# Optimization experiments

Measured on AMD Instinct MI355X. Metric: run time of the kernel, lower is better.

The kernel has to match this reference:

```python
import jax, jax.numpy as jnp
import numpy as np

EPS = 1e-5
MAX_NORM = 1.0 - EPS
K = 16
ALPHA = 0.1
TAU = 0.1  # softmax temperature in forward


def project(x):
    # enforce ||x|| < 1 on the Poincare ball
    n = jnp.clip(jnp.linalg.norm(x, axis=-1, keepdims=True), EPS, None)
    return x / jnp.maximum(n / MAX_NORM, 1.0)


def mobius_add(u, v):
    c = 1.0
    dot_uv = jnp.sum(u * v, axis=-1, keepdims=True)
    nu = jnp.clip(jnp.sum(u * u, axis=-1, keepdims=True), 0.0, MAX_NORM ** 2)
    nv = jnp.clip(jnp.sum(v * v, axis=-1, keepdims=True), 0.0, MAX_NORM ** 2)
    num = (1 + 2 * c * dot_uv + c * nv) * u + (1 - c * nu) * v
    den = 1 + 2 * c * dot_uv + c * c * nu * nv
    return project(num / jnp.clip(den, EPS, None))


def exp_map(x, v):
    # sqrt_c = 1
    vn = jnp.clip(jnp.linalg.norm(v, axis=-1, keepdims=True), EPS, None)
    second = jnp.tanh(vn / 2.0) * v / vn
    return mobius_add(x, second)


def poincare_cdist(q, mem):
    # q: [B, M], mem: [N, M] -> [B, N] geodesic distances (c=1)
    qn = jnp.clip(jnp.sum(q * q, axis=-1), 0.0, MAX_NORM ** 2)          # [B]
    mn = jnp.clip(jnp.sum(mem * mem, axis=-1), 0.0, MAX_NORM ** 2)      # [N]
    # ||q - m||^2 expanded via gram matrix (same math as diff-based form)
    dist_sq = jnp.clip(jnp.sum(q * q, axis=-1)[:, None] + jnp.sum(mem * mem, axis=-1)[None, :]
                       - 2.0 * q @ mem.T, 0.0, None)                     # [B, N]
    den = (1.0 - qn)[:, None] * (1.0 - mn)[None, :]
    x = 2.0 * dist_sq / jnp.clip(den, EPS, None)
    return jnp.arccosh(1.0 + x)


def layernorm(x, g, b):
    mu = jnp.mean(x, axis=-1, keepdims=True)
    var = jnp.mean((x - mu) ** 2, axis=-1, keepdims=True)
    return (x - mu) / jnp.sqrt(var + 1e-5) * g + b


def setup_inputs() -> dict:
    key = jax.random.key(0)
    ks = jax.random.split(key, 10)
    B, S, H, M, N = 32, 2048, 1024, 128, 500000
    hidden_states = jax.random.normal(ks[0], (B, S, H), dtype=jnp.float32)
    W1 = jax.random.normal(ks[1], (H, M), dtype=jnp.float32) * 0.02
    b1 = jnp.zeros((M,), dtype=jnp.float32)
    ln_g = jnp.ones((M,), dtype=jnp.float32)
    ln_b = jnp.zeros((M,), dtype=jnp.float32)
    W2 = jax.random.normal(ks[2], (M, M), dtype=jnp.float32) * 0.02
    b2 = jnp.zeros((M,), dtype=jnp.float32)
    q_origin = jnp.zeros((1, M), dtype=jnp.float32)
    memory = project(jax.random.normal(ks[3], (N, M), dtype=jnp.float32) * 0.3)
    Wp = jax.random.normal(ks[4], (M, H), dtype=jnp.float32) * 0.02
    bp = jnp.zeros((H,), dtype=jnp.float32)
    return {"hidden_states": hidden_states, "W1": W1, "b1": b1, "ln_g": ln_g,
            "ln_b": ln_b, "W2": W2, "b2": b2, "q_origin": q_origin,
            "memory": memory, "Wp": Wp, "bp": bp}


def reference(hidden_states, W1, b1, ln_g, ln_b, W2, b2, q_origin, memory, Wp, bp):
    B, S, H = hidden_states.shape
    # query network on mean-pooled hidden states
    pooled = jnp.mean(hidden_states, axis=1)                  # [B, H]
    h = pooled @ W1 + b1                                      # [B, M]
    h = jax.nn.gelu(layernorm(h, ln_g, ln_b), approximate=False)
    tangent = h @ W2 + b2                                     # [B, M]
    origin = project(jnp.broadcast_to(q_origin, (B, q_origin.shape[-1])))
    query = exp_map(origin, tangent)                          # [B, M] on ball
    # geodesic kNN over the memory bank
    dists = poincare_cdist(query, memory)                     # [B, N]
    neg_top, idx = jax.lax.top_k(-dists, K)                   # smallest K
    top_d = -neg_top                                          # [B, K]
    neighbors = memory[idx]                                   # [B, K, M]
    w = jax.nn.softmax(-top_d / TAU, axis=-1)                 # [B, K]
    retrieved = jnp.einsum('bk,bkm->bm', w, neighbors)        # [B, M]
    force = retrieved @ Wp + bp                               # [B, H]
    return hidden_states + ALPHA * force[:, None, :]
```

## Files before the change

### kernel.cpp

```cpp
#include <hip/hip_runtime.h>
#include <float.h>
#include <math.h>

#define B_ 32
#define S_ 2048
#define H_ 1024
#define M_ 128
#define N_ 500000
#define KK 16
#define KK2 32
#define ALPHA_ 0.1f
#define TAU_ 0.1f
#define EPS_ 1e-5f
#define MAX_NORM_ 0.99999f
#define MAXN2_ (MAX_NORM_ * MAX_NORM_)
#define SC_ 64
#define RPB_ 256
#define NBLK_ ((N_ + RPB_ - 1) / RPB_)
#define WIN_ 2048
#define NWIN_ ((N_ + WIN_ - 1) / WIN_)
#define NPAD_ (NWIN_ * WIN_)

typedef __attribute__((ext_vector_type(8))) short short8;
typedef __attribute__((ext_vector_type(4))) float f32x4;

__device__ __forceinline__ unsigned short to_bf16(float x) {
    unsigned u = __float_as_uint(x);
    return (unsigned short)((u + 0x7FFFu + ((u >> 16) & 1u)) >> 16);
}

__global__ __launch_bounds__(256) void k1_pool(const float* __restrict__ hid,
                                               float* __restrict__ pp) {
    int bid = blockIdx.x;
    int b = bid >> 6, sc = bid & 63;
    const float4* h4 = (const float4*)hid + (((size_t)(b * S_ + sc * (S_ / SC_))) << 8) + threadIdx.x;
    float4 a0 = {0.f, 0.f, 0.f, 0.f}, a1 = a0, a2 = a0, a3 = a0;
    #pragma unroll
    for (int s = 0; s < S_ / SC_; s += 4) {
        float4 v0 = h4[(size_t)(s + 0) << 8];
        float4 v1 = h4[(size_t)(s + 1) << 8];
        float4 v2 = h4[(size_t)(s + 2) << 8];
        float4 v3 = h4[(size_t)(s + 3) << 8];
        a0.x += v0.x; a0.y += v0.y; a0.z += v0.z; a0.w += v0.w;
        a1.x += v1.x; a1.y += v1.y; a1.z += v1.z; a1.w += v1.w;
        a2.x += v2.x; a2.y += v2.y; a2.z += v2.z; a2.w += v2.w;
        a3.x += v3.x; a3.y += v3.y; a3.z += v3.z; a3.w += v3.w;
    }
    float4 acc;
    acc.x = (a0.x + a1.x) + (a2.x + a3.x);
    acc.y = (a0.y + a1.y) + (a2.y + a3.y);
    acc.z = (a0.z + a1.z) + (a2.z + a3.z);
    acc.w = (a0.w + a1.w) + (a2.w + a3.w);
    ((float4*)pp)[(size_t)(b * SC_ + sc) * 256 + threadIdx.x] = acc;
}

__device__ __forceinline__ float bred256(float v, volatile float* red, int tid) {
    red[tid] = v;
    __syncthreads();
    if (tid < 64) {
        float x = red[tid] + red[tid + 64] + red[tid + 128] + red[tid + 192];
        #pragma unroll
        for (int off = 32; off >= 1; off >>= 1) x += __shfl_down(x, off);
        if (tid == 0) red[0] = x;
    }
    __syncthreads();
    float r = red[0];
    __syncthreads();
    return r;
}

__global__ __launch_bounds__(256) void k2_query(const float* __restrict__ pp,
                         const float* __restrict__ W1,
                         const float* __restrict__ b1, const float* __restrict__ ln_g,
                         const float* __restrict__ ln_b, const float* __restrict__ W2,
                         const float* __restrict__ b2, const float* __restrict__ qorig,
                         float* __restrict__ query, float* __restrict__ qstats) {
    __shared__ float pooled[H_];
    __shared__ float red[256];
    __shared__ float hv[M_];
    int b = blockIdx.x, tid = threadIdx.x;
    #pragma unroll
    for (int j = 0; j < H_ / 256; ++j) {
        int h = tid + j * 256;
        float s = 0.f;
        for (int sc = 0; sc < SC_; ++sc) s += pp[(size_t)(b * SC_ + sc) * H_ + h];
        pooled[h] = s * (1.0f / (float)S_);
    }
    __syncthreads();
    int m = tid & 127, half = tid >> 7;
    {
        const float* wcol = W1 + m;
        int k0 = half * (H_ / 2);
        float a0 = 0.f, a1 = 0.f, a2 = 0.f, a3 = 0.f;
        #pragma unroll 4
        for (int k = k0; k < k0 + H_ / 2; k += 4) {
            a0 = fmaf(pooled[k + 0], wcol[(k + 0) * M_], a0);
            a1 = fmaf(pooled[k + 1], wcol[(k + 1) * M_], a1);
            a2 = fmaf(pooled[k + 2], wcol[(k + 2) * M_], a2);
            a3 = fmaf(pooled[k + 3], wcol[(k + 3) * M_], a3);
        }
        red[tid] = (a0 + a1) + (a2 + a3);
    }
    __syncthreads();
    float x = (tid < M_) ? (red[m] + red[m + 128] + b1[m]) : 0.f;
    __syncthreads();
    float mu = bred256(x, red, tid) * (1.0f / (float)M_);
    float dmu = (tid < M_) ? (x - mu) : 0.f;
    float var = bred256(dmu * dmu, red, tid) * (1.0f / (float)M_);
    float lg = (tid < M_) ? ln_g[m] : 0.f;
    float lb = (tid < M_) ? ln_b[m] : 0.f;
    float xh = dmu * rsqrtf(var + 1e-5f) * lg + lb;
    float g = 0.5f * xh * (1.0f + erff(xh * 0.70710678f));
    if (tid < M_) hv[m] = g;
    __syncthreads();
    float t = 0.f;
    if (tid < M_) {
        const float* wcol = W2 + m;
        float a0 = b2[m], a1 = 0.f, a2 = 0.f, a3 = 0.f;
        #pragma unroll 4
        for (int k = 0; k < M_; k += 4) {
            a0 = fmaf(hv[k + 0], wcol[(k + 0) * M_], a0);
            a1 = fmaf(hv[k + 1], wcol[(k + 1) * M_], a1);
            a2 = fmaf(hv[k + 2], wcol[(k + 2) * M_], a2);
            a3 = fmaf(hv[k + 3], wcol[(k + 3) * M_], a3);
        }
        t = (a0 + a1) + (a2 + a3);
    }
    float o = (tid < M_) ? qorig[m] : 0.f;
    float on2 = bred256(o * o, red, tid);
    float on = fmaxf(sqrtf(on2), EPS_);
    float osc = 1.0f / fmaxf(on / MAX_NORM_, 1.0f);
    float u = o * osc;
    float vn2 = bred256(t * t, red, tid);
    float vn = fmaxf(sqrtf(vn2), EPS_);
    float sec = tanhf(vn * 0.5f) * t / vn;
    float dot_uv = bred256(u * sec, red, tid);
    float nu = fminf(fmaxf(bred256(u * u, red, tid), 0.f), MAXN2_);
    float nv = fminf(fmaxf(bred256(sec * sec, red, tid), 0.f), MAXN2_);
    float num = (1.0f + 2.0f * dot_uv + nv) * u + (1.0f - nu) * sec;
    float den = 1.0f + 2.0f * dot_uv + nu * nv;
    float r = num / fmaxf(den, EPS_);
    float rn2 = bred256(r * r, red, tid);
    float rn = fmaxf(sqrtf(rn2), EPS_);
    float rsc = 1.0f / fmaxf(rn / MAX_NORM_, 1.0f);
    float q = r * rsc;
    if (tid < M_) query[b * M_ + m] = q;
    float qq = bred256(q * q, red, tid);
    if (tid == 0) {
        qstats[b * 2 + 0] = qq;
        float qn = fminf(fmaxf(qq, 0.f), MAXN2_);
        qstats[b * 2 + 1] = 1.0f - qn;
    }
}

__global__ __launch_bounds__(256, 3) void k3_scores(const float* __restrict__ mem,
                                                    const float* __restrict__ query,
                                                    const float* __restrict__ qstats,
                                                    unsigned short* __restrict__ keyplane) {
    __shared__ unsigned short key_lds[B_][264];
    __shared__ float mm_lds[256];
    __shared__ float qq_s[B_], omq_s[B_];
    int tid = threadIdx.x, bid = blockIdx.x;
    int wave = tid >> 6, lane = tid & 63;
    int l15 = lane & 15, lk = lane >> 4;

    if (tid < B_) { qq_s[tid] = qstats[tid * 2]; omq_s[tid] = qstats[tid * 2 + 1]; }

    short8 bfrag[2][4];
    #pragma unroll
    for (int bg = 0; bg < 2; ++bg) {
        #pragma unroll
        for (int kt = 0; kt < 4; ++kt) {
            int batch = bg * 16 + l15;
            const float4* qp = (const float4*)(query + batch * M_ + kt * 32 + lk * 8);
            float4 lo = qp[0], hi = qp[1];
            short8 f;
            f[0] = (short)to_bf16(lo.x); f[1] = (short)to_bf16(lo.y);
            f[2] = (short)to_bf16(lo.z); f[3] = (short)to_bf16(lo.w);
            f[4] = (short)to_bf16(hi.x); f[5] = (short)to_bf16(hi.y);
            f[6] = (short)to_bf16(hi.z); f[7] = (short)to_bf16(hi.w);
            bfrag[bg][kt] = f;
        }
    }

    int passbase = bid * RPB_;
    f32x4 acc[4][2];
    #pragma unroll
    for (int rg = 0; rg < 4; ++rg)
        #pragma unroll
        for (int bg = 0; bg < 2; ++bg)
            acc[rg][bg] = (f32x4){0.f, 0.f, 0.f, 0.f};
    float mmp[4] = {0.f, 0.f, 0.f, 0.f};

    #pragma unroll
    for (int rg = 0; rg < 4; ++rg) {
        int r = passbase + wave * 64 + rg * 16 + l15;
        const float4* mp = (const float4*)(mem + (size_t)((r < N_) ? r : 0) * M_);
        #pragma unroll
        for (int kt = 0; kt < 4; ++kt) {
            float4 lo = mp[kt * 8 + lk * 2];
            float4 hi = mp[kt * 8 + lk * 2 + 1];
            mmp[rg] = fmaf(lo.x, lo.x, fmaf(lo.y, lo.y, fmaf(lo.z, lo.z, fmaf(lo.w, lo.w, mmp[rg]))));
            mmp[rg] = fmaf(hi.x, hi.x, fmaf(hi.y, hi.y, fmaf(hi.z, hi.z, fmaf(hi.w, hi.w, mmp[rg]))));
            short8 af;
            af[0] = (short)to_bf16(lo.x); af[1] = (short)to_bf16(lo.y);
            af[2] = (short)to_bf16(lo.z); af[3] = (short)to_bf16(lo.w);
            af[4] = (short)to_bf16(hi.x); af[5] = (short)to_bf16(hi.y);
            af[6] = (short)to_bf16(hi.z); af[7] = (short)to_bf16(hi.w);
            acc[rg][0] = __builtin_amdgcn_mfma_f32_16x16x32_bf16(af, bfrag[0][kt], acc[rg][0], 0, 0, 0);
            acc[rg][1] = __builtin_amdgcn_mfma_f32_16x16x32_bf16(af, bfrag[1][kt], acc[rg][1], 0, 0, 0);
        }
    }
    #pragma unroll
    for (int rg = 0; rg < 4; ++rg) {
        float v = mmp[rg] + __shfl_xor(mmp[rg], 16);
        v += __shfl_xor(v, 32);
        if (lane < 16) mm_lds[wave * 64 + rg * 16 + l15] = v;
    }
    __syncthreads();

    #pragma unroll
    for (int rg = 0; rg < 4; ++rg) {
        #pragma unroll
        for (int bg = 0; bg < 2; ++bg) {
            #pragma unroll
            for (int reg = 0; reg < 4; ++reg) {
                int row_local = wave * 64 + rg * 16 + lk * 4 + reg;
                int batch = bg * 16 + l15;
                float dot = acc[rg][bg][reg];
                float mmv = mm_lds[row_local];
                float mn = fminf(mmv, MAXN2_);
                float dsq = fmaxf(qq_s[batch] + mmv - 2.0f * dot, 0.f);
                float t = dsq / fmaxf(omq_s[batch] * (1.0f - mn), EPS_);
                key_lds[batch][row_local] = to_bf16(t);
            }
        }
    }
    __syncthreads();

    {
        int batch = tid >> 3, chunk = tid & 7;
        int rbase = passbase + chunk * 32;
        unsigned short* dstp = keyplane + (size_t)batch * NPAD_ + rbase;
        #pragma unroll
        for (int i = 0; i < 4; ++i) {
            int gr = rbase + i * 8;
            uint4 v = *(const uint4*)&key_lds[batch][chunk * 32 + i * 8];
            if (gr + 8 <= N_) {
                *(uint4*)(dstp + i * 8) = v;
            } else {
                for (int t = 0; t < 8; ++t)
                    if (gr + t < N_) dstp[i * 8 + t] = key_lds[batch][chunk * 32 + i * 8 + t];
            }
        }
    }
}

__global__ __launch_bounds__(256, 4) void k4_sel(const unsigned short* __restrict__ keyplane,
                                                 unsigned* __restrict__ cand_key) {
    int win = blockIdx.x >> 2, quad = blockIdx.x & 3;
    int wave = threadIdx.x >> 6, lane = threadIdx.x & 63;
    int base = win * WIN_;
    #pragma unroll 1
    for (int j = 0; j < 2; ++j) {
        int b = quad * 8 + wave * 2 + j;
        const uint4* kp = (const uint4*)(keyplane + (size_t)b * NPAD_ + base);
        unsigned keys[32];
        #pragma unroll
        for (int i = 0; i < 4; ++i) {
            uint4 v = kp[lane + i * 64];
            int rl0 = (lane + i * 64) * 8;
            int pos = base + rl0;
            unsigned s[8];
            s[0] = v.x & 0xFFFFu; s[1] = v.x >> 16;
            s[2] = v.y & 0xFFFFu; s[3] = v.y >> 16;
            s[4] = v.z & 0xFFFFu; s[5] = v.z >> 16;
            s[6] = v.w & 0xFFFFu; s[7] = v.w >> 16;
            #pragma unroll
            for (int t = 0; t < 8; ++t)
                keys[i * 8 + t] = (pos + t < N_) ? ((s[t] << 11) | (unsigned)(rl0 + t))
                                                 : 0xFFFFFFFFu;
        }
        for (int k = 0; k < KK; ++k) {
            unsigned m = keys[0];
            #pragma unroll
            for (int i = 1; i < 32; ++i) m = min(m, keys[i]);
            #pragma unroll
            for (int off = 32; off >= 1; off >>= 1)
                m = min(m, (unsigned)__shfl_xor((int)m, off));
            if (lane == 0) cand_key[((size_t)win * B_ + b) * KK + k] = m;
            #pragma unroll
            for (int i = 0; i < 32; ++i)
                if (keys[i] == m) keys[i] = 0xFFFFFFFFu;
        }
    }
}

__global__ void k45_retrieve(const unsigned* __restrict__ cand_key,
                             const float* __restrict__ mem, const float* __restrict__ query,
                             const float* __restrict__ qstats,
                             float* __restrict__ retbuf) {
    __shared__ unsigned tv[256 * KK];
    __shared__ int ti[256 * KK];
    __shared__ unsigned mv[64 * KK];
    __shared__ int mi[64 * KK];
    __shared__ int top32_s[KK2];
    __shared__ float q_s[M_];
    __shared__ float d_s[KK2];
    __shared__ float w_s[KK];
    __shared__ int idx_s[KK];
    int b = blockIdx.x, tid = threadIdx.x;

    unsigned val[KK]; int idx[KK];
    #pragma unroll
    for (int i = 0; i < KK; ++i) { val[i] = 0xFFFFFFFFu; idx[i] = 0; }
    int nc = NWIN_ * KK;
    for (int c = tid; c < nc; c += 256) {
        int g = c >> 4, k = c & 15;
        unsigned v = cand_key[((size_t)g * B_ + b) * KK + k];
        int id = g * WIN_ + (int)(v & 2047u);
        if (v < val[KK - 1]) {
            val[KK - 1] = v; idx[KK - 1] = id;
            #pragma unroll
            for (int j = KK - 1; j > 0; --j) {
                if (val[j] < val[j - 1]) {
                    unsigned tvv = val[j]; val[j] = val[j - 1]; val[j - 1] = tvv;
                    int tii = idx[j]; idx[j] = idx[j - 1]; idx[j - 1] = tii;
                }
            }
        }
    }
    if (tid < M_) q_s[tid] = query[b * M_ + tid];
    #pragma unroll
    for (int i = 0; i < KK; ++i) { tv[tid * KK + i] = val[i]; ti[tid * KK + i] = idx[i]; }
    __syncthreads();

    if (tid < 64) {
        #pragma unroll
        for (int i = 0; i < KK; ++i) { val[i] = 0xFFFFFFFFu; idx[i] = 0; }
        for (int t = tid * 4; t < tid * 4 + 4; ++t) {
            for (int i = 0; i < KK; ++i) {
                unsigned v = tv[t * KK + i]; int id = ti[t * KK + i];
                if (v >= val[KK - 1]) break;
                val[KK - 1] = v; idx[KK - 1] = id;
                #pragma unroll
                for (int j = KK - 1; j > 0; --j) {
                    if (val[j] < val[j - 1]) {
                        unsigned tvv = val[j]; val[j] = val[j - 1]; val[j - 1] = tvv;
                        int tii = idx[j]; idx[j] = idx[j - 1]; idx[j - 1] = tii;
                    }
                }
            }
        }
        #pragma unroll
        for (int i = 0; i < KK; ++i) { mv[tid * KK + i] = val[i]; mi[tid * KK + i] = idx[i]; }
        int h = 0;
        for (int k = 0; k < KK2; ++k) {
            unsigned cv = (h < KK) ? mv[tid * KK + h] : 0xFFFFFFFFu;
            int ci = (h < KK) ? mi[tid * KK + h] : 0;
            unsigned bestv = cv; int bestl = tid;
            #pragma unroll
            for (int off = 32; off >= 1; off >>= 1) {
                unsigned ov = (unsigned)__shfl_down((int)bestv, off);
                int ol = __shfl_down(bestl, off);
                if (ov < bestv) { bestv = ov; bestl = ol; }
            }
            bestl = __shfl(bestl, 0);
            if (tid == bestl) {
                top32_s[k] = (ci < 0) ? 0 : ((ci >= N_) ? (N_ - 1) : ci);
                h++;
            }
        }
    }
    __syncthreads();

    float qq = qstats[b * 2], omq = qstats[b * 2 + 1];
    int wave = tid >> 6, lane = tid & 63;
    for (int ii = wave; ii < KK2; ii += 4) {
        const float* mr = mem + (size_t)top32_s[ii] * M_;
        float a0 = mr[lane], a1 = mr[lane + 64];
        float p = q_s[lane] * a0 + q_s[lane + 64] * a1;
        float mm = a0 * a0 + a1 * a1;
        #pragma unroll
        for (int off = 32; off >= 1; off >>= 1) {
            p += __shfl_down(p, off);
            mm += __shfl_down(mm, off);
        }
        if (lane == 0) {
            float dsq = fmaxf(qq + mm - 2.0f * p, 0.f);
            float mn = fminf(mm, MAXN2_);
            float t = dsq / fmaxf(omq * (1.0f - mn), EPS_);
            d_s[ii] = acoshf(1.0f + 2.0f * t);
        }
    }
    __syncthreads();
    if (tid == 0) {
        bool used[KK2];
        for (int i = 0; i < KK2; ++i) used[i] = false;
        float seld[KK];
        for (int k = 0; k < KK; ++k) {
            float bd = FLT_MAX; int bi = -1;
            for (int i = 0; i < KK2; ++i) {
                if (used[i]) continue;
                if (d_s[i] < bd || (d_s[i] == bd && (bi < 0 || top32_s[i] < top32_s[bi]))) {
                    bd = d_s[i]; bi = i;
                }
            }
            used[bi] = true; seld[k] = bd; idx_s[k] = top32_s[bi];
        }
        float dmin = seld[0];
        for (int i = 1; i < KK; ++i) dmin = fminf(dmin, seld[i]);
        float Z = 0.f;
        for (int i = 0; i < KK; ++i) {
            float w = expf((dmin - seld[i]) * (1.0f / TAU_));
            w_s[i] = w; Z += w;
        }
        float iZ = 1.0f / Z;
        for (int i = 0; i < KK; ++i) w_s[i] *= iZ;
    }
    __syncthreads();
    if (tid < M_) {
        float r = 0.f;
        #pragma unroll
        for (int i = 0; i < KK; ++i) r = fmaf(w_s[i], mem[(size_t)idx_s[i] * M_ + tid], r);
        retbuf[b * M_ + tid] = r;
    }
}

__global__ __launch_bounds__(256) void k5_force(const float* __restrict__ retbuf,
                                                const float* __restrict__ Wp,
                                                const float* __restrict__ bp,
                                                float* __restrict__ force) {
    __shared__ float r_s[M_];
    int b = blockIdx.x >> 2, quad = blockIdx.x & 3;
    int tid = threadIdx.x;
    if (tid < M_) r_s[tid] = retbuf[b * M_ + tid];
    __syncthreads();
    int h = quad * 256 + tid;
    const float* wp = Wp + h;
    float a0 = bp[h], a1 = 0.f, a2 = 0.f, a3 = 0.f;
    #pragma unroll 8
    for (int k = 0; k < M_; k += 4) {
        a0 = fmaf(r_s[k + 0], wp[(k + 0) * H_], a0);
        a1 = fmaf(r_s[k + 1], wp[(k + 1) * H_], a1);
        a2 = fmaf(r_s[k + 2], wp[(k + 2) * H_], a2);
        a3 = fmaf(r_s[k + 3], wp[(k + 3) * H_], a3);
    }
    force[b * H_ + h] = (a0 + a1) + (a2 + a3);
}

__global__ __launch_bounds__(256) void k6_out(const float* __restrict__ hid,
                                              const float* __restrict__ force,
                                              float* __restrict__ out) {
    const float4* h4 = (const float4*)hid;
    const float4* f4 = (const float4*)force;
    float4* o4 = (float4*)out;
    int n4 = B_ * S_ * H_ / 4;
    for (int i = blockIdx.x * blockDim.x + threadIdx.x; i < n4; i += gridDim.x * blockDim.x) {
        int b = i >> 19;
        float4 hv = h4[i];
        float4 fv = f4[(b << 8) + (i & 255)];
        float4 ov;
        ov.x = fmaf(ALPHA_, fv.x, hv.x);
        ov.y = fmaf(ALPHA_, fv.y, hv.y);
        ov.z = fmaf(ALPHA_, fv.z, hv.z);
        ov.w = fmaf(ALPHA_, fv.w, hv.w);
        o4[i] = ov;
    }
}

extern "C" void kernel_launch(void* const* d_in, const int* in_sizes, int n_in,
                              void* d_out, int out_size, void* d_ws, size_t ws_size,
                              hipStream_t stream) {
    const float* hid    = (const float*)d_in[0];
    const float* W1     = (const float*)d_in[1];
    const float* b1     = (const float*)d_in[2];
    const float* ln_g   = (const float*)d_in[3];
    const float* ln_b   = (const float*)d_in[4];
    const float* W2     = (const float*)d_in[5];
    const float* b2     = (const float*)d_in[6];
    const float* qorig  = (const float*)d_in[7];
    const float* mem    = (const float*)d_in[8];
    const float* Wp     = (const float*)d_in[9];
    const float* bp     = (const float*)d_in[10];
    float* outp = (float*)d_out;

    char* ws = (char*)d_ws;
    size_t off = 0;
    float* pp = (float*)(ws + off);        off += (size_t)B_ * SC_ * H_ * 4;
    float* query = (float*)(ws + off);     off += (size_t)B_ * M_ * 4;
    float* qstats = (float*)(ws + off);    off += (size_t)B_ * 2 * 4;
    off = (off + 255) & ~(size_t)255;
    unsigned short* keyplane = (unsigned short*)(ws + off); off += (size_t)B_ * NPAD_ * 2;
    off = (off + 255) & ~(size_t)255;
    unsigned* cand_key = (unsigned*)(ws + off); off += (size_t)NWIN_ * B_ * KK * 4;
    float* retbuf = (float*)(ws + off);    off += (size_t)B_ * M_ * 4;
    float* force = (float*)(ws + off);     off += (size_t)B_ * H_ * 4;
    (void)ws_size; (void)in_sizes; (void)n_in; (void)out_size;

    hipLaunchKernelGGL(k1_pool, dim3(B_ * SC_), dim3(256), 0, stream, hid, pp);
    hipLaunchKernelGGL(k2_query, dim3(B_), dim3(256), 0, stream, pp, W1, b1, ln_g, ln_b,
                       W2, b2, qorig, query, qstats);
    hipLaunchKernelGGL(k3_scores, dim3(NBLK_), dim3(256), 0, stream, mem, query, qstats, keyplane);
    hipLaunchKernelGGL(k4_sel, dim3(NWIN_ * 4), dim3(256), 0, stream, keyplane, cand_key);
    hipLaunchKernelGGL(k45_retrieve, dim3(B_), dim3(256), 0, stream, cand_key,
                       mem, query, qstats, retbuf);
    hipLaunchKernelGGL(k5_force, dim3(B_ * 4), dim3(256), 0, stream, retbuf, Wp, bp, force);
    hipLaunchKernelGGL(k6_out, dim3(2048), dim3(256), 0, stream, hid, force, outp);
}
```

Measured before the change: 379.7 us.

## Fuse per-block top-K selection into scoring kernel and fuse retrieve with force

Each scoring block now runs its own wave-level top-16 selection over its 256 rows for every batch, straight from LDS. This removes the bf16 key-plane write and its re-read by a separate selection kernel. The retrieve kernel also absorbs the Wp projection, dropping one launch and the retbuf round-trip. In exchange, the candidate buffer grows to one entry set per 256-row block instead of per 2048-row window. The merge kernel therefore scans roughly eight times more candidates, and each batch's merge is repeated in four blocks.

```diff
diff --git a/kernel.cpp b/kernel.cpp
--- a/kernel.cpp
+++ b/kernel.cpp
@@ -17,9 +17,6 @@
 #define SC_ 64
 #define RPB_ 256
 #define NBLK_ ((N_ + RPB_ - 1) / RPB_)
-#define WIN_ 2048
-#define NWIN_ ((N_ + WIN_ - 1) / WIN_)
-#define NPAD_ (NWIN_ * WIN_)
 
 typedef __attribute__((ext_vector_type(8))) short short8;
 typedef __attribute__((ext_vector_type(4))) float f32x4;
@@ -153,10 +150,10 @@
     }
 }
 
-__global__ __launch_bounds__(256, 3) void k3_scores(const float* __restrict__ mem,
-                                                    const float* __restrict__ query,
-                                                    const float* __restrict__ qstats,
-                                                    unsigned short* __restrict__ keyplane) {
+__global__ __launch_bounds__(256, 3) void k3_scoresel(const float* __restrict__ mem,
+                                                      const float* __restrict__ query,
+                                                      const float* __restrict__ qstats,
+                                                      unsigned* __restrict__ cand_key) {
     __shared__ unsigned short key_lds[B_][264];
     __shared__ float mm_lds[256];
     __shared__ float qq_s[B_], omq_s[B_];
@@ -238,68 +235,38 @@
     }
     __syncthreads();
 
-    {
-        int batch = tid >> 3, chunk = tid & 7;
-        int rbase = passbase + chunk * 32;
-        unsigned short* dstp = keyplane + (size_t)batch * NPAD_ + rbase;
-        #pragma unroll
-        for (int i = 0; i < 4; ++i) {
-            int gr = rbase + i * 8;
-            uint4 v = *(const uint4*)&key_lds[batch][chunk * 32 + i * 8];
-            if (gr + 8 <= N_) {
-                *(uint4*)(dstp + i * 8) = v;
-            } else {
-                for (int t = 0; t < 8; ++t)
-                    if (gr + t < N_) dstp[i * 8 + t] = key_lds[batch][chunk * 32 + i * 8 + t];
-            }
-        }
-    }
-}
-
-__global__ __launch_bounds__(256, 4) void k4_sel(const unsigned short* __restrict__ keyplane,
-                                                 unsigned* __restrict__ cand_key) {
-    int win = blockIdx.x >> 2, quad = blockIdx.x & 3;
-    int wave = threadIdx.x >> 6, lane = threadIdx.x & 63;
-    int base = win * WIN_;
     #pragma unroll 1
-    for (int j = 0; j < 2; ++j) {
-        int b = quad * 8 + wave * 2 + j;
-        const uint4* kp = (const uint4*)(keyplane + (size_t)b * NPAD_ + base);
-        unsigned keys[32];
-        #pragma unroll
-        for (int i = 0; i < 4; ++i) {
-            uint4 v = kp[lane + i * 64];
-            int rl0 = (lane + i * 64) * 8;
-            int pos = base + rl0;
-            unsigned s[8];
-            s[0] = v.x & 0xFFFFu; s[1] = v.x >> 16;
-            s[2] = v.y & 0xFFFFu; s[3] = v.y >> 16;
-            s[4] = v.z & 0xFFFFu; s[5] = v.z >> 16;
-            s[6] = v.w & 0xFFFFu; s[7] = v.w >> 16;
-            #pragma unroll
-            for (int t = 0; t < 8; ++t)
-                keys[i * 8 + t] = (pos + t < N_) ? ((s[t] << 11) | (unsigned)(rl0 + t))
-                                                 : 0xFFFFFFFFu;
+    for (int j = 0; j < 8; ++j) {
+        int batch = wave * 8 + j;
+        unsigned k0, k1, k2, k3;
+        {
+            int rl0 = lane, rl1 = lane + 64, rl2 = lane + 128, rl3 = lane + 192;
+            unsigned s0 = key_lds[batch][rl0], s1 = key_lds[batch][rl1];
+            unsigned s2 = key_lds[batch][rl2], s3 = key_lds[batch][rl3];
+            k0 = (passbase + rl0 < N_) ? ((s0 << 8) | (unsigned)rl0) : 0xFFFFFFFFu;
+            k1 = (passbase + rl1 < N_) ? ((s1 << 8) | (unsigned)rl1) : 0xFFFFFFFFu;
+            k2 = (passbase + rl2 < N_) ? ((s2 << 8) | (unsigned)rl2) : 0xFFFFFFFFu;
+            k3 = (passbase + rl3 < N_) ? ((s3 << 8) | (unsigned)rl3) : 0xFFFFFFFFu;
         }
         for (int k = 0; k < KK; ++k) {
-            unsigned m = keys[0];
-            #pragma unroll
-            for (int i = 1; i < 32; ++i) m = min(m, keys[i]);
+            unsigned m = min(min(k0, k1), min(k2, k3));
             #pragma unroll
             for (int off = 32; off >= 1; off >>= 1)
                 m = min(m, (unsigned)__shfl_xor((int)m, off));
-            if (lane == 0) cand_key[((size_t)win * B_ + b) * KK + k] = m;
-            #pragma unroll
-            for (int i = 0; i < 32; ++i)
-                if (keys[i] == m) keys[i] = 0xFFFFFFFFu;
-        }
-    }
-}
-
-__global__ void k45_retrieve(const unsigned* __restrict__ cand_key,
-                             const float* __restrict__ mem, const float* __restrict__ query,
-                             const float* __restrict__ qstats,
-                             float* __restrict__ retbuf) {
+            if (lane == 0) cand_key[((size_t)bid * B_ + batch) * KK + k] = m;
+            if (k0 == m) k0 = 0xFFFFFFFFu;
+            if (k1 == m) k1 = 0xFFFFFFFFu;
+            if (k2 == m) k2 = 0xFFFFFFFFu;
+            if (k3 == m) k3 = 0xFFFFFFFFu;
+        }
+    }
+}
+
+__global__ void k45_force(const unsigned* __restrict__ cand_key,
+                          const float* __restrict__ mem, const float* __restrict__ query,
+                          const float* __restrict__ qstats,
+                          const float* __restrict__ Wp, const float* __restrict__ bp,
+                          float* __restrict__ force) {
     __shared__ unsigned tv[256 * KK];
     __shared__ int ti[256 * KK];
     __shared__ unsigned mv[64 * KK];
@@ -309,16 +276,17 @@
     __shared__ float d_s[KK2];
     __shared__ float w_s[KK];
     __shared__ int idx_s[KK];
-    int b = blockIdx.x, tid = threadIdx.x;
+    __shared__ float ret_s[M_];
+    int b = blockIdx.x >> 2, quad = blockIdx.x & 3, tid = threadIdx.x;
 
     unsigned val[KK]; int idx[KK];
     #pragma unroll
     for (int i = 0; i < KK; ++i) { val[i] = 0xFFFFFFFFu; idx[i] = 0; }
-    int nc = NWIN_ * KK;
+    int nc = NBLK_ * KK;
     for (int c = tid; c < nc; c += 256) {
         int g = c >> 4, k = c & 15;
         unsigned v = cand_key[((size_t)g * B_ + b) * KK + k];
-        int id = g * WIN_ + (int)(v & 2047u);
+        int id = g * RPB_ + (int)(v & 255u);
         if (v < val[KK - 1]) {
             val[KK - 1] = v; idx[KK - 1] = id;
             #pragma unroll
@@ -423,30 +391,22 @@
         float r = 0.f;
         #pragma unroll
         for (int i = 0; i < KK; ++i) r = fmaf(w_s[i], mem[(size_t)idx_s[i] * M_ + tid], r);
-        retbuf[b * M_ + tid] = r;
-    }
-}
-
-__global__ __launch_bounds__(256) void k5_force(const float* __restrict__ retbuf,
-                                                const float* __restrict__ Wp,
-                                                const float* __restrict__ bp,
-                                                float* __restrict__ force) {
-    __shared__ float r_s[M_];
-    int b = blockIdx.x >> 2, quad = blockIdx.x & 3;
-    int tid = threadIdx.x;
-    if (tid < M_) r_s[tid] = retbuf[b * M_ + tid];
-    __syncthreads();
-    int h = quad * 256 + tid;
-    const float* wp = Wp + h;
-    float a0 = bp[h], a1 = 0.f, a2 = 0.f, a3 = 0.f;
-    #pragma unroll 8
-    for (int k = 0; k < M_; k += 4) {
-        a0 = fmaf(r_s[k + 0], wp[(k + 0) * H_], a0);
-        a1 = fmaf(r_s[k + 1], wp[(k + 1) * H_], a1);
-        a2 = fmaf(r_s[k + 2], wp[(k + 2) * H_], a2);
-        a3 = fmaf(r_s[k + 3], wp[(k + 3) * H_], a3);
-    }
-    force[b * H_ + h] = (a0 + a1) + (a2 + a3);
+        ret_s[tid] = r;
+    }
+    __syncthreads();
+    {
+        int h = quad * 256 + tid;
+        const float* wp = Wp + h;
+        float a0 = bp[h], a1 = 0.f, a2 = 0.f, a3 = 0.f;
+        #pragma unroll 8
+        for (int k = 0; k < M_; k += 4) {
+            a0 = fmaf(ret_s[k + 0], wp[(k + 0) * H_], a0);
+            a1 = fmaf(ret_s[k + 1], wp[(k + 1) * H_], a1);
+            a2 = fmaf(ret_s[k + 2], wp[(k + 2) * H_], a2);
+            a3 = fmaf(ret_s[k + 3], wp[(k + 3) * H_], a3);
+        }
+        force[b * H_ + h] = (a0 + a1) + (a2 + a3);
+    }
 }
 
 __global__ __launch_bounds__(256) void k6_out(const float* __restrict__ hid,
@@ -491,20 +451,15 @@
     float* query = (float*)(ws + off);     off += (size_t)B_ * M_ * 4;
     float* qstats = (float*)(ws + off);    off += (size_t)B_ * 2 * 4;
     off = (off + 255) & ~(size_t)255;
-    unsigned short* keyplane = (unsigned short*)(ws + off); off += (size_t)B_ * NPAD_ * 2;
-    off = (off + 255) & ~(size_t)255;
-    unsigned* cand_key = (unsigned*)(ws + off); off += (size_t)NWIN_ * B_ * KK * 4;
-    float* retbuf = (float*)(ws + off);    off += (size_t)B_ * M_ * 4;
+    unsigned* cand_key = (unsigned*)(ws + off); off += (size_t)NBLK_ * B_ * KK * 4;
     float* force = (float*)(ws + off);     off += (size_t)B_ * H_ * 4;
     (void)ws_size; (void)in_sizes; (void)n_in; (void)out_size;
 
     hipLaunchKernelGGL(k1_pool, dim3(B_ * SC_), dim3(256), 0, stream, hid, pp);
     hipLaunchKernelGGL(k2_query, dim3(B_), dim3(256), 0, stream, pp, W1, b1, ln_g, ln_b,
                        W2, b2, qorig, query, qstats);
-    hipLaunchKernelGGL(k3_scores, dim3(NBLK_), dim3(256), 0, stream, mem, query, qstats, keyplane);
-    hipLaunchKernelGGL(k4_sel, dim3(NWIN_ * 4), dim3(256), 0, stream, keyplane, cand_key);
-    hipLaunchKernelGGL(k45_retrieve, dim3(B_), dim3(256), 0, stream, cand_key,
-                       mem, query, qstats, retbuf);
-    hipLaunchKernelGGL(k5_force, dim3(B_ * 4), dim3(256), 0, stream, retbuf, Wp, bp, force);
+    hipLaunchKernelGGL(k3_scoresel, dim3(NBLK_), dim3(256), 0, stream, mem, query, qstats, cand_key);
+    hipLaunchKernelGGL(k45_force, dim3(B_ * 4), dim3(256), 0, stream, cand_key,
+                       mem, query, qstats, Wp, bp, force);
     hipLaunchKernelGGL(k6_out, dim3(2048), dim3(256), 0, stream, hid, force, outp);
 }
```

Result: slower. 499.6 us (+31.6%).
